# Kernel optimization log

Measured on AMD Instinct MI355X. Metric: run time of the kernel, lower is better.

Reference implementation:

```python
import jax, jax.numpy as jnp
import numpy as np

B, S, D, E, H = 4, 2048, 1024, 8, 4096  # batch, seq, d_model, n_experts, ffn hidden (4*d_model)


def setup_inputs() -> dict:
    key = jax.random.key(0)
    ks = jax.random.split(key, 4)
    s = 0.02  # init scale
    return {
        "x": jax.random.normal(ks[0], (B, S, D), dtype=jnp.float32),
        "router_w": jax.random.normal(ks[1], (E, D), dtype=jnp.float32) * s,
        "router_b": jnp.zeros((E,), dtype=jnp.float32),
        "w1": jax.random.normal(ks[2], (E, D, H), dtype=jnp.float32) * s,
        "b1": jnp.zeros((E, H), dtype=jnp.float32),
        "w2": jax.random.normal(ks[3], (E, H, D), dtype=jnp.float32) * s,
        "b2": jnp.zeros((E, D), dtype=jnp.float32),
        "top_k": 2,
    }


def reference(x, router_w, router_b, w1, b1, w2, b2, top_k):
    # Router logits [B, S, E]
    logits = jnp.einsum('bsd,ed->bse', x, router_w) + router_b
    # Top-k selection; scatter top-k logits into a -inf tensor, then softmax
    # => gate weight is exactly 0 for non-selected experts.
    top_v, top_i = jax.lax.top_k(logits, top_k)           # [B, S, k]
    sel = jax.nn.one_hot(top_i, logits.shape[-1], dtype=bool).any(axis=-2)  # [B, S, E]
    gate = jax.nn.softmax(jnp.where(sel, logits, -jnp.inf), axis=-1)        # [B, S, E]

    # Dense sum over experts (mathematically identical to the masked
    # gather/scatter loop since non-selected gates are exactly 0).
    out = jnp.zeros_like(x)
    for e in range(w1.shape[0]):  # small fixed expert loop keeps peak memory low
        h = jax.nn.relu(x @ w1[e] + b1[e])        # [B, S, H]
        out = out + (h @ w2[e] + b2[e]) * gate[..., e:e + 1]
    return out
```

## Files before the change

kernel.cpp:

```cpp
#include <hip/hip_runtime.h>
#include <hip/hip_bf16.h>

#define NTOK   8192
#define DMODEL 1024
#define NEXP   8
#define HFFN   4096
#define NSLOT  16384
#define MAXWL  136

typedef __bf16 bf16x8 __attribute__((ext_vector_type(8)));
typedef float  f32x4  __attribute__((ext_vector_type(4)));
typedef unsigned short u16;
typedef u16 u16x8 __attribute__((ext_vector_type(8)));

typedef const __attribute__((address_space(1))) void* gas_ptr;
typedef __attribute__((address_space(3))) void* las_ptr;

__device__ inline u16 f2b(float f) {
  __hip_bfloat16 h = __float2bfloat16(f);
  return *reinterpret_cast<u16*>(&h);
}
__device__ inline float b2f(u16 u) {
  unsigned int v = ((unsigned int)u) << 16;
  return *reinterpret_cast<float*>(&v);
}

__global__ void router_k(const float* __restrict__ x, const float* __restrict__ rw,
                         const float* __restrict__ rb, int* __restrict__ tok_e,
                         float* __restrict__ tok_g, int* __restrict__ counts) {
  __shared__ int h[NEXP];
  int tid = threadIdx.x;
  if (tid < NEXP) h[tid] = 0;
  __syncthreads();
  int wave = tid >> 6, lane = tid & 63;
  int t = blockIdx.x * 4 + wave;
  const float* xr = x + (size_t)t * DMODEL;
  float acc[NEXP];
#pragma unroll
  for (int e = 0; e < NEXP; e++) acc[e] = 0.f;
#pragma unroll
  for (int i = 0; i < 4; i++) {
    int d = i * 256 + lane * 4;
    float4 xv = *(const float4*)(xr + d);
#pragma unroll
    for (int e = 0; e < NEXP; e++) {
      float4 wv = *(const float4*)(rw + (size_t)e * DMODEL + d);
      acc[e] += xv.x * wv.x + xv.y * wv.y + xv.z * wv.z + xv.w * wv.w;
    }
  }
#pragma unroll
  for (int e = 0; e < NEXP; e++) {
#pragma unroll
    for (int off = 32; off > 0; off >>= 1) acc[e] += __shfl_xor(acc[e], off);
  }
  if (lane == 0) {
    float lg[NEXP];
#pragma unroll
    for (int e = 0; e < NEXP; e++) lg[e] = acc[e] + rb[e];
    int e0 = 0;
#pragma unroll
    for (int e = 1; e < NEXP; e++) if (lg[e] > lg[e0]) e0 = e;
    int e1 = (e0 == 0) ? 1 : 0;
#pragma unroll
    for (int e = 0; e < NEXP; e++) if (e != e0 && lg[e] > lg[e1]) e1 = e;
    float ex = expf(lg[e1] - lg[e0]);
    float g0 = 1.f / (1.f + ex);
    float g1 = ex / (1.f + ex);
    tok_e[2 * t]     = e0;  tok_e[2 * t + 1] = e1;
    tok_g[2 * t]     = g0;  tok_g[2 * t + 1] = g1;
    atomicAdd(&h[e0], 1);
    atomicAdd(&h[e1], 1);
  }
  __syncthreads();
  if (tid < NEXP && h[tid]) atomicAdd(&counts[tid], h[tid]);
}

__global__ void offsets_k(const int* __restrict__ counts, int* __restrict__ offsets,
                          int* __restrict__ wl) {
  if (threadIdx.x == 0) {
    int s = 0;
    for (int e = 0; e < NEXP; e++) { offsets[e] = s; s += counts[e]; }
    offsets[NEXP] = s;
    int n = 0;
    for (int e = 0; e < NEXP; e++)
      for (int t = 0; t * 128 < counts[e]; ++t) wl[n++] = (e << 16) | t;
    for (int i = n; i < MAXWL; ++i) wl[i] = -1;
  }
}

__global__ void assign_k(const int* __restrict__ tok_e, int* __restrict__ cursors,
                         const int* __restrict__ offsets, int* __restrict__ row_tok,
                         int* __restrict__ slot_of) {
  __shared__ int h[NEXP], base[NEXP];
  int tid = threadIdx.x;
  if (tid < NEXP) h[tid] = 0;
  __syncthreads();
  int t = blockIdx.x * 256 + tid;
  int e0 = tok_e[2 * t], e1 = tok_e[2 * t + 1];
  int r0 = atomicAdd(&h[e0], 1);
  int r1 = atomicAdd(&h[e1], 1);
  __syncthreads();
  if (tid < NEXP) base[tid] = atomicAdd(&cursors[tid], h[tid]);
  __syncthreads();
  int s0 = offsets[e0] + base[e0] + r0;
  int s1 = offsets[e1] + base[e1] + r1;
  row_tok[s0] = t;  slot_of[2 * t] = s0;
  row_tok[s1] = t;  slot_of[2 * t + 1] = s1;
}

__global__ void gather_k(const float* __restrict__ x, const int* __restrict__ row_tok,
                         u16* __restrict__ xbg) {
  int idx = blockIdx.x * 256 + threadIdx.x;
  int s = idx >> 8;
  int c = (idx & 255) * 4;
  int t = row_tok[s];
  float4 v = *(const float4*)(x + (size_t)t * DMODEL + c);
  ushort4 o;
  o.x = f2b(v.x); o.y = f2b(v.y); o.z = f2b(v.z); o.w = f2b(v.w);
  *(ushort4*)(xbg + (size_t)s * DMODEL + c) = o;
}

__global__ void wtrans_k(const float* __restrict__ src, u16* __restrict__ dst,
                         int R, int C) {
  __shared__ u16 tile[64][72];
  int e = blockIdx.z;
  int r0 = blockIdx.x * 64, c0 = blockIdx.y * 64;
  int tid = threadIdx.x;
  int tr = tid >> 2, tc = (tid & 3) * 16;
  const float* sp = src + (size_t)e * R * C + (size_t)(r0 + tr) * C + c0 + tc;
#pragma unroll
  for (int i = 0; i < 16; i += 4) {
    float4 v = *(const float4*)(sp + i);
    tile[tr][tc + i]     = f2b(v.x);
    tile[tr][tc + i + 1] = f2b(v.y);
    tile[tr][tc + i + 2] = f2b(v.z);
    tile[tr][tc + i + 3] = f2b(v.w);
  }
  __syncthreads();
  u16* dbase = dst + (size_t)e * R * C;
#pragma unroll
  for (int it = 0; it < 2; ++it) {
    int oc  = it * 32 + (tid >> 3);
    int seg = (tid & 7) * 8;
    u16x8 o;
#pragma unroll
    for (int j = 0; j < 8; ++j) o[j] = tile[seg + j][oc];
    *(u16x8*)(dbase + (size_t)(c0 + oc) * R + r0 + seg) = o;
  }
}

template <int KTOT, int KCHUNK, int NTOT, int NY, bool RELU, bool BIAS>
__global__ __launch_bounds__(256, 4) void moe_gemm_k(
    const u16* __restrict__ A, const u16* __restrict__ Bt,
    const float* __restrict__ bias, u16* __restrict__ Out,
    const int* __restrict__ counts, const int* __restrict__ offsets,
    const int* __restrict__ wl) {
  __shared__ __align__(16) u16 Als[128 * 32];
  __shared__ __align__(16) u16 Bls[128 * 32];

  int nwg = gridDim.x;
  int lid = blockIdx.x;
  int orig = (lid & 7) * (nwg >> 3) + (lid >> 3);
  int kq   = orig / (MAXWL * NY);
  int r1   = orig - kq * (MAXWL * NY);
  int xp   = r1 / (NY * 2);
  int r2   = r1 - xp * (NY * 2);
  int xt = (xp << 1) | (r2 & 1);
  int y  = r2 >> 1;
  int w = wl[xt];
  if (w < 0) return;
  int e   = w >> 16;
  int tr0 = (w & 0xffff) << 7;
  int cnt = counts[e];
  int seg = offsets[e];
  int n0  = y << 7;

  int tid = threadIdx.x;
  int wid = tid >> 6, lane = tid & 63;
  int wm = wid >> 1, wn = wid & 1;
  int l15 = lane & 15, lhi = lane >> 4;

  int co = (((tid & 3) ^ ((tid >> 3) & 3)) << 3) + kq * KCHUNK;
  const u16* gA0 = A + (size_t)(seg + tr0 + (tid >> 2)) * KTOT + co;
  const u16* gA1 = gA0 + (size_t)64 * KTOT;
  const u16* Bte = Bt + (size_t)e * NTOT * KTOT;
  const u16* gB0 = Bte + (size_t)(n0 + (tid >> 2)) * KTOT + co;
  const u16* gB1 = gB0 + (size_t)64 * KTOT;
  char* Ab = (char*)Als;
  char* Bb = (char*)Bls;
  int sdst = wid << 10;

  int xsw = ((lhi ^ ((l15 >> 1) & 3)) << 4);
  int aoff = (wm * 64 + l15) * 64 + xsw;
  int boff = (wn * 64 + l15) * 64 + xsw;

  f32x4 acc[4][4] = {};
  constexpr int NT = KCHUNK / 32;
  for (int kt = 0; kt < NT; ++kt) {
    int kb = kt * 32;
    __builtin_amdgcn_global_load_lds((gas_ptr)(gA0 + kb), (las_ptr)(Ab + sdst), 16, 0, 0);
    __builtin_amdgcn_global_load_lds((gas_ptr)(gA1 + kb), (las_ptr)(Ab + 4096 + sdst), 16, 0, 0);
    __builtin_amdgcn_global_load_lds((gas_ptr)(gB0 + kb), (las_ptr)(Bb + sdst), 16, 0, 0);
    __builtin_amdgcn_global_load_lds((gas_ptr)(gB1 + kb), (las_ptr)(Bb + 4096 + sdst), 16, 0, 0);
    asm volatile("s_waitcnt vmcnt(0)" ::: "memory");
    __builtin_amdgcn_s_barrier();

    bf16x8 af[4], bv[4];
#pragma unroll
    for (int m = 0; m < 4; ++m) af[m] = *(const bf16x8*)(Ab + aoff + m * 1024);
#pragma unroll
    for (int n = 0; n < 4; ++n) bv[n] = *(const bf16x8*)(Bb + boff + n * 1024);
#pragma unroll
    for (int m = 0; m < 4; ++m)
#pragma unroll
      for (int n = 0; n < 4; ++n)
        acc[m][n] = __builtin_amdgcn_mfma_f32_16x16x32_bf16(af[m], bv[n], acc[m][n], 0, 0, 0);
    __builtin_amdgcn_s_barrier();
  }

  u16* outp = Out + (size_t)kq * ((size_t)NSLOT * NTOT);

  int cb = n0 + wn * 64 + l15;
  float bs4[4] = {0.f, 0.f, 0.f, 0.f};
  if (BIAS) {
    const float* bias_e = bias + (size_t)e * NTOT;
#pragma unroll
    for (int n = 0; n < 4; ++n) bs4[n] = bias_e[cb + n * 16];
  }
  int rb0 = tr0 + wm * 64 + lhi * 4;
#pragma unroll
  for (int m = 0; m < 4; ++m) {
#pragma unroll
    for (int r = 0; r < 4; ++r) {
      int gi = rb0 + m * 16 + r;
      if (gi >= cnt) continue;
      size_t orow = (size_t)(seg + gi) * NTOT + cb;
#pragma unroll
      for (int n = 0; n < 4; ++n) {
        float v = acc[m][n][r] + bs4[n];
        if (RELU) v = fmaxf(v, 0.f);
        outp[orow + n * 16] = f2b(v);
      }
    }
  }
}

__global__ void combine_k(const u16* __restrict__ Y, const int* __restrict__ slot_of,
                          const int* __restrict__ tok_e, const float* __restrict__ tok_g,
                          const float* __restrict__ b2, float* __restrict__ out) {
  int t = blockIdx.x;
  int d = threadIdx.x * 4;
  int s0 = slot_of[2 * t], s1 = slot_of[2 * t + 1];
  int e0 = tok_e[2 * t],  e1 = tok_e[2 * t + 1];
  float g0 = tok_g[2 * t], g1 = tok_g[2 * t + 1];
  const u16* Y1 = Y + (size_t)NSLOT * DMODEL;
  ushort4 a0 = *(const ushort4*)(Y  + (size_t)s0 * DMODEL + d);
  ushort4 a1 = *(const ushort4*)(Y1 + (size_t)s0 * DMODEL + d);
  ushort4 c0 = *(const ushort4*)(Y  + (size_t)s1 * DMODEL + d);
  ushort4 c1 = *(const ushort4*)(Y1 + (size_t)s1 * DMODEL + d);
  float4 b20 = *(const float4*)(b2 + (size_t)e0 * DMODEL + d);
  float4 b21 = *(const float4*)(b2 + (size_t)e1 * DMODEL + d);
  float4 o;
  o.x = g0 * (b2f(a0.x) + b2f(a1.x) + b20.x) + g1 * (b2f(c0.x) + b2f(c1.x) + b21.x);
  o.y = g0 * (b2f(a0.y) + b2f(a1.y) + b20.y) + g1 * (b2f(c0.y) + b2f(c1.y) + b21.y);
  o.z = g0 * (b2f(a0.z) + b2f(a1.z) + b20.z) + g1 * (b2f(c0.z) + b2f(c1.z) + b21.z);
  o.w = g0 * (b2f(a0.w) + b2f(a1.w) + b20.w) + g1 * (b2f(c0.w) + b2f(c1.w) + b21.w);
  *(float4*)(out + (size_t)t * DMODEL + d) = o;
}

extern "C" void kernel_launch(void* const* d_in, const int* in_sizes, int n_in,
                              void* d_out, int out_size, void* d_ws, size_t ws_size,
                              hipStream_t stream) {
  const float* x  = (const float*)d_in[0];
  const float* rw = (const float*)d_in[1];
  const float* rb = (const float*)d_in[2];
  const float* w1 = (const float*)d_in[3];
  const float* b1 = (const float*)d_in[4];
  const float* w2 = (const float*)d_in[5];
  const float* b2 = (const float*)d_in[6];

  char* ws = (char*)d_ws;
  size_t o = 0;
  u16* w1t = (u16*)(ws + o); o += (size_t)NEXP * HFFN * DMODEL * 2;
  u16* w2t = (u16*)(ws + o); o += (size_t)NEXP * HFFN * DMODEL * 2;
  u16* xbg = (u16*)(ws + o); o += (size_t)(NSLOT + 256) * DMODEL * 2;
  u16* hc  = (u16*)(ws + o); o += (size_t)(NSLOT + 256) * HFFN * 2;
  u16* yp  = (u16*)w1t;
  int*   tok_e   = (int*)(ws + o);   o += NTOK * 2 * sizeof(int);
  float* tok_g   = (float*)(ws + o); o += NTOK * 2 * sizeof(float);
  int*   slot_of = (int*)(ws + o);   o += NTOK * 2 * sizeof(int);
  int*   row_tok = (int*)(ws + o);   o += NSLOT * sizeof(int);
  int*   meta    = (int*)(ws + o);   o += 32 * sizeof(int);
  int*   wl      = (int*)(ws + o);   o += MAXWL * sizeof(int);
  int* counts  = meta;
  int* cursors = meta + 8;
  int* offsets = meta + 16;

  hipMemsetAsync(meta, 0, 64, stream);
  router_k<<<NTOK / 4, 256, 0, stream>>>(x, rw, rb, tok_e, tok_g, counts);
  offsets_k<<<1, 64, 0, stream>>>(counts, offsets, wl);
  assign_k<<<NTOK / 256, 256, 0, stream>>>(tok_e, cursors, offsets, row_tok, slot_of);
  gather_k<<<NSLOT, 256, 0, stream>>>(x, row_tok, xbg);
  wtrans_k<<<dim3(DMODEL / 64, HFFN / 64, NEXP), 256, 0, stream>>>(w1, w1t, DMODEL, HFFN);
  wtrans_k<<<dim3(HFFN / 64, DMODEL / 64, NEXP), 256, 0, stream>>>(w2, w2t, HFFN, DMODEL);

  moe_gemm_k<DMODEL, DMODEL, HFFN, HFFN / 128, true, true>
      <<<MAXWL * (HFFN / 128), 256, 0, stream>>>(
          xbg, w1t, b1, hc, counts, offsets, wl);
  moe_gemm_k<HFFN, HFFN / 2, DMODEL, DMODEL / 128, false, false>
      <<<MAXWL * (DMODEL / 128) * 2, 256, 0, stream>>>(
          hc, w2t, nullptr, yp, counts, offsets, wl);

  combine_k<<<NTOK, 256, 0, stream>>>(yp, slot_of, tok_e, tok_g, b2, (float*)d_out);
}
```

Before: 522.2 us.

## Use 256x256 tiles with 8 waves and a double-buffered interleaved LDS pipeline

Both expert GEMMs move from 128x128 tiles with 4 waves and a single LDS buffer to 256x256 tiles with 512 threads. The new kernel double-buffers A and B in LDS (128 KB total) and overlaps the quarter-tile global-to-LDS loads with MFMA groups, using fine-grained vmcnt waits and setprio. The expert work list is rebuilt for 256-row chunks. The aim is to raise arithmetic intensity and hide load latency. In exchange, the grid is much smaller, only two blocks can be resident per CU, and register pressure rises.

```diff
diff --git a/kernel.cpp b/kernel.cpp
--- a/kernel.cpp
+++ b/kernel.cpp
@@ -6,7 +6,7 @@
 #define NEXP   8
 #define HFFN   4096
 #define NSLOT  16384
-#define MAXWL  136
+#define MAXWL2 72
 
 typedef __bf16 bf16x8 __attribute__((ext_vector_type(8)));
 typedef float  f32x4  __attribute__((ext_vector_type(4)));
@@ -83,8 +83,8 @@
     offsets[NEXP] = s;
     int n = 0;
     for (int e = 0; e < NEXP; e++)
-      for (int t = 0; t * 128 < counts[e]; ++t) wl[n++] = (e << 16) | t;
-    for (int i = n; i < MAXWL; ++i) wl[i] = -1;
+      for (int t = 0; t * 256 < counts[e]; ++t) wl[n++] = (e << 16) | t;
+    for (int i = n; i < MAXWL2; ++i) wl[i] = -1;
   }
 }
 
@@ -150,19 +150,19 @@
 }
 
 template <int KTOT, int KCHUNK, int NTOT, int NY, bool RELU, bool BIAS>
-__global__ __launch_bounds__(256, 4) void moe_gemm_k(
+__global__ __launch_bounds__(512, 2) void moe_gemm8_k(
     const u16* __restrict__ A, const u16* __restrict__ Bt,
     const float* __restrict__ bias, u16* __restrict__ Out,
     const int* __restrict__ counts, const int* __restrict__ offsets,
     const int* __restrict__ wl) {
-  __shared__ __align__(16) u16 Als[128 * 32];
-  __shared__ __align__(16) u16 Bls[128 * 32];
+  __shared__ __align__(16) u16 Als[2 * 256 * 64];
+  __shared__ __align__(16) u16 Bls[2 * 256 * 64];
 
   int nwg = gridDim.x;
   int lid = blockIdx.x;
   int orig = (lid & 7) * (nwg >> 3) + (lid >> 3);
-  int kq   = orig / (MAXWL * NY);
-  int r1   = orig - kq * (MAXWL * NY);
+  int kq   = orig / (MAXWL2 * NY);
+  int r1   = orig - kq * (MAXWL2 * NY);
   int xp   = r1 / (NY * 2);
   int r2   = r1 - xp * (NY * 2);
   int xt = (xp << 1) | (r2 & 1);
@@ -170,52 +170,152 @@
   int w = wl[xt];
   if (w < 0) return;
   int e   = w >> 16;
-  int tr0 = (w & 0xffff) << 7;
+  int tr0 = (w & 0xffff) << 8;
   int cnt = counts[e];
   int seg = offsets[e];
-  int n0  = y << 7;
-
-  int tid = threadIdx.x;
-  int wid = tid >> 6, lane = tid & 63;
-  int wm = wid >> 1, wn = wid & 1;
+  int n0  = y << 8;
+
+  int t = threadIdx.x;
+  int wid = t >> 6, lane = t & 63;
+  int wm = wid >> 2, wn = wid & 3;
   int l15 = lane & 15, lhi = lane >> 4;
-
-  int co = (((tid & 3) ^ ((tid >> 3) & 3)) << 3) + kq * KCHUNK;
-  const u16* gA0 = A + (size_t)(seg + tr0 + (tid >> 2)) * KTOT + co;
-  const u16* gA1 = gA0 + (size_t)64 * KTOT;
-  const u16* Bte = Bt + (size_t)e * NTOT * KTOT;
-  const u16* gB0 = Bte + (size_t)(n0 + (tid >> 2)) * KTOT + co;
-  const u16* gB1 = gB0 + (size_t)64 * KTOT;
-  char* Ab = (char*)Als;
-  char* Bb = (char*)Bls;
-  int sdst = wid << 10;
-
-  int xsw = ((lhi ^ ((l15 >> 1) & 3)) << 4);
-  int aoff = (wm * 64 + l15) * 64 + xsw;
-  int boff = (wn * 64 + l15) * 64 + xsw;
-
-  f32x4 acc[4][4] = {};
-  constexpr int NT = KCHUNK / 32;
-  for (int kt = 0; kt < NT; ++kt) {
-    int kb = kt * 32;
-    __builtin_amdgcn_global_load_lds((gas_ptr)(gA0 + kb), (las_ptr)(Ab + sdst), 16, 0, 0);
-    __builtin_amdgcn_global_load_lds((gas_ptr)(gA1 + kb), (las_ptr)(Ab + 4096 + sdst), 16, 0, 0);
-    __builtin_amdgcn_global_load_lds((gas_ptr)(gB0 + kb), (las_ptr)(Bb + sdst), 16, 0, 0);
-    __builtin_amdgcn_global_load_lds((gas_ptr)(gB1 + kb), (las_ptr)(Bb + 4096 + sdst), 16, 0, 0);
-    asm volatile("s_waitcnt vmcnt(0)" ::: "memory");
-    __builtin_amdgcn_s_barrier();
-
-    bf16x8 af[4], bv[4];
-#pragma unroll
-    for (int m = 0; m < 4; ++m) af[m] = *(const bf16x8*)(Ab + aoff + m * 1024);
-#pragma unroll
-    for (int n = 0; n < 4; ++n) bv[n] = *(const bf16x8*)(Bb + boff + n * 1024);
-#pragma unroll
-    for (int m = 0; m < 4; ++m)
-#pragma unroll
-      for (int n = 0; n < 4; ++n)
-        acc[m][n] = __builtin_amdgcn_mfma_f32_16x16x32_bf16(af[m], bv[n], acc[m][n], 0, 0, 0);
-    __builtin_amdgcn_s_barrier();
+  int l7 = l15 & 7;
+
+  int co = (((t & 7) ^ ((t >> 3) & 7)) << 3) + kq * KCHUNK;
+  int rl = t >> 3;
+  const u16* Ab0 = A + (size_t)(seg + tr0) * KTOT + co;
+  const u16* Bb0 = Bt + (size_t)e * NTOT * KTOT + (size_t)n0 * KTOT + co;
+  const u16 *gA1[2], *gA3[2], *gB1[2], *gB2[2];
+  int dA1[2], dA3[2], dB1[2], dB2[2];
+#pragma unroll
+  for (int j = 0; j < 2; ++j) {
+    int rA1 = j * 128 + rl;
+    int rA3 = 64 + j * 128 + rl;
+    int rlj = j * 64 + rl;
+    int rB1 = (rlj & 31) + ((rlj >> 5) << 6);
+    int rB2 = rB1 + 32;
+    gA1[j] = Ab0 + (size_t)rA1 * KTOT;  dA1[j] = rA1 * 128 + (t & 7) * 16;
+    gA3[j] = Ab0 + (size_t)rA3 * KTOT;  dA3[j] = rA3 * 128 + (t & 7) * 16;
+    gB1[j] = Bb0 + (size_t)rB1 * KTOT;  dB1[j] = rB1 * 128 + (t & 7) * 16;
+    gB2[j] = Bb0 + (size_t)rB2 * KTOT;  dB2[j] = rB2 * 128 + (t & 7) * 16;
+  }
+  char* AL = (char*)Als;
+  char* BL = (char*)Bls;
+
+  auto stA1 = [&](int b, int kt) {
+#pragma unroll
+    for (int j = 0; j < 2; ++j)
+      __builtin_amdgcn_global_load_lds((gas_ptr)(gA1[j] + kt * 64),
+          (las_ptr)(AL + b * 32768 + dA1[j]), 16, 0, 0);
+  };
+  auto stA3 = [&](int b, int kt) {
+#pragma unroll
+    for (int j = 0; j < 2; ++j)
+      __builtin_amdgcn_global_load_lds((gas_ptr)(gA3[j] + kt * 64),
+          (las_ptr)(AL + b * 32768 + dA3[j]), 16, 0, 0);
+  };
+  auto stB1 = [&](int b, int kt) {
+#pragma unroll
+    for (int j = 0; j < 2; ++j)
+      __builtin_amdgcn_global_load_lds((gas_ptr)(gB1[j] + kt * 64),
+          (las_ptr)(BL + b * 32768 + dB1[j]), 16, 0, 0);
+  };
+  auto stB2 = [&](int b, int kt) {
+#pragma unroll
+    for (int j = 0; j < 2; ++j)
+      __builtin_amdgcn_global_load_lds((gas_ptr)(gB2[j] + kt * 64),
+          (las_ptr)(BL + b * 32768 + dB2[j]), 16, 0, 0);
+  };
+
+  bf16x8 a[4][2], b[4][2];
+  f32x4 acc[8][4] = {};
+
+  auto rdA = [&](int bf, int grp) {
+    const char* base = AL + bf * 32768;
+    int rbase = wm * 128 + grp * 64 + l15;
+#pragma unroll
+    for (int mm = 0; mm < 4; ++mm) {
+      int row = rbase + mm * 16;
+#pragma unroll
+      for (int ks = 0; ks < 2; ++ks)
+        a[mm][ks] = *(const bf16x8*)(base + row * 128 + (((ks << 2) + lhi) ^ l7) * 16);
+    }
+  };
+  auto rdB = [&](int bf, int grp) {
+    const char* base = BL + bf * 32768;
+    int rbase = wn * 64 + grp * 32 + l15;
+#pragma unroll
+    for (int nn = 0; nn < 2; ++nn) {
+      int row = rbase + nn * 16;
+#pragma unroll
+      for (int ks = 0; ks < 2; ++ks)
+        b[grp * 2 + nn][ks] = *(const bf16x8*)(base + row * 128 + (((ks << 2) + lhi) ^ l7) * 16);
+    }
+  };
+  auto mf = [&](int gm, int gn) {
+    __builtin_amdgcn_s_setprio(1);
+#pragma unroll
+    for (int mm = 0; mm < 4; ++mm)
+#pragma unroll
+      for (int nn = 0; nn < 2; ++nn)
+#pragma unroll
+        for (int ks = 0; ks < 2; ++ks)
+          acc[gm * 4 + mm][gn * 2 + nn] = __builtin_amdgcn_mfma_f32_16x16x32_bf16(
+              a[mm][ks], b[gn * 2 + nn][ks], acc[gm * 4 + mm][gn * 2 + nn], 0, 0, 0);
+    __builtin_amdgcn_s_setprio(0);
+  };
+
+  constexpr int NT = KCHUNK / 64;
+
+  stA1(0, 0); stB1(0, 0); stB2(0, 0); stA3(0, 0);
+  stA1(1, 1);
+  asm volatile("s_waitcnt vmcnt(6)" ::: "memory");
+  __builtin_amdgcn_s_barrier();
+  __builtin_amdgcn_sched_barrier(0);
+
+  for (int tt = 0; tt < NT; ++tt) {
+    int cur = tt & 1, nxt = cur ^ 1;
+    bool s1 = (tt + 1 < NT), s2 = (tt + 2 < NT);
+
+    rdA(cur, 0); rdB(cur, 0);
+    if (s1) stB1(nxt, tt + 1);
+    __builtin_amdgcn_s_barrier();
+    asm volatile("s_waitcnt lgkmcnt(0)" ::: "memory");
+    __builtin_amdgcn_sched_barrier(0);
+    mf(0, 0);
+    if (s1) asm volatile("s_waitcnt vmcnt(6)" ::: "memory");
+    else    asm volatile("s_waitcnt vmcnt(2)" ::: "memory");
+    __builtin_amdgcn_s_barrier();
+    __builtin_amdgcn_sched_barrier(0);
+
+    rdB(cur, 1);
+    if (s1) stB2(nxt, tt + 1);
+    __builtin_amdgcn_s_barrier();
+    asm volatile("s_waitcnt lgkmcnt(0)" ::: "memory");
+    __builtin_amdgcn_sched_barrier(0);
+    mf(0, 1);
+    if (s1) asm volatile("s_waitcnt vmcnt(6)" ::: "memory");
+    else    asm volatile("s_waitcnt vmcnt(0)" ::: "memory");
+    __builtin_amdgcn_s_barrier();
+    __builtin_amdgcn_sched_barrier(0);
+
+    rdA(cur, 1);
+    if (s1) stA3(nxt, tt + 1);
+    __builtin_amdgcn_s_barrier();
+    asm volatile("s_waitcnt lgkmcnt(0)" ::: "memory");
+    __builtin_amdgcn_sched_barrier(0);
+    mf(1, 1);
+    if (s1) asm volatile("s_waitcnt vmcnt(6)" ::: "memory");
+    __builtin_amdgcn_s_barrier();
+    __builtin_amdgcn_sched_barrier(0);
+
+    if (s2) stA1(cur, tt + 2);
+    __builtin_amdgcn_s_barrier();
+    mf(1, 0);
+    if (s2)      asm volatile("s_waitcnt vmcnt(6)" ::: "memory");
+    else if (s1) asm volatile("s_waitcnt vmcnt(4)" ::: "memory");
+    __builtin_amdgcn_s_barrier();
+    __builtin_amdgcn_sched_barrier(0);
   }
 
   u16* outp = Out + (size_t)kq * ((size_t)NSLOT * NTOT);
@@ -225,21 +325,21 @@
   if (BIAS) {
     const float* bias_e = bias + (size_t)e * NTOT;
 #pragma unroll
-    for (int n = 0; n < 4; ++n) bs4[n] = bias_e[cb + n * 16];
-  }
-  int rb0 = tr0 + wm * 64 + lhi * 4;
-#pragma unroll
-  for (int m = 0; m < 4; ++m) {
+    for (int nn = 0; nn < 4; ++nn) bs4[nn] = bias_e[cb + nn * 16];
+  }
+  int rb0 = tr0 + wm * 128 + lhi * 4;
+#pragma unroll
+  for (int mm = 0; mm < 8; ++mm) {
 #pragma unroll
     for (int r = 0; r < 4; ++r) {
-      int gi = rb0 + m * 16 + r;
+      int gi = rb0 + mm * 16 + r;
       if (gi >= cnt) continue;
       size_t orow = (size_t)(seg + gi) * NTOT + cb;
 #pragma unroll
-      for (int n = 0; n < 4; ++n) {
-        float v = acc[m][n][r] + bs4[n];
+      for (int nn = 0; nn < 4; ++nn) {
+        float v = acc[mm][nn][r] + bs4[nn];
         if (RELU) v = fmaxf(v, 0.f);
-        outp[orow + n * 16] = f2b(v);
+        outp[orow + nn * 16] = f2b(v);
       }
     }
   }
@@ -291,7 +391,7 @@
   int*   slot_of = (int*)(ws + o);   o += NTOK * 2 * sizeof(int);
   int*   row_tok = (int*)(ws + o);   o += NSLOT * sizeof(int);
   int*   meta    = (int*)(ws + o);   o += 32 * sizeof(int);
-  int*   wl      = (int*)(ws + o);   o += MAXWL * sizeof(int);
+  int*   wl      = (int*)(ws + o);   o += MAXWL2 * sizeof(int);
   int* counts  = meta;
   int* cursors = meta + 8;
   int* offsets = meta + 16;
@@ -304,11 +404,11 @@
   wtrans_k<<<dim3(DMODEL / 64, HFFN / 64, NEXP), 256, 0, stream>>>(w1, w1t, DMODEL, HFFN);
   wtrans_k<<<dim3(HFFN / 64, DMODEL / 64, NEXP), 256, 0, stream>>>(w2, w2t, HFFN, DMODEL);
 
-  moe_gemm_k<DMODEL, DMODEL, HFFN, HFFN / 128, true, true>
-      <<<MAXWL * (HFFN / 128), 256, 0, stream>>>(
+  moe_gemm8_k<DMODEL, DMODEL, HFFN, HFFN / 256, true, true>
+      <<<MAXWL2 * (HFFN / 256), 512, 0, stream>>>(
           xbg, w1t, b1, hc, counts, offsets, wl);
-  moe_gemm_k<HFFN, HFFN / 2, DMODEL, DMODEL / 128, false, false>
-      <<<MAXWL * (DMODEL / 128) * 2, 256, 0, stream>>>(
+  moe_gemm8_k<HFFN, HFFN / 2, DMODEL, DMODEL / 256, false, false>
+      <<<MAXWL2 * (DMODEL / 256) * 2, 512, 0, stream>>>(
           hc, w2t, nullptr, yp, counts, offsets, wl);
 
   combine_k<<<NTOK, 256, 0, stream>>>(yp, slot_of, tok_e, tok_g, b2, (float*)d_out);
```

Result: slower. 533.6 us (+2.2%).
